# Optimization experiments

Hardware: AMD Instinct MI355X
Metric: run time of the kernel (lower is better)

Reference implementation:

```python
import jax, jax.numpy as jnp
import numpy as np

B, T, C = 4, 2048, 1024
H = 16
D = C // H  # head_dim = 64

def setup_inputs() -> dict:
    key = jax.random.key(0)
    k1, k2, k3 = jax.random.split(key, 3)
    s = 1.0 / np.sqrt(C)
    x = jax.random.normal(k1, (B, T, C), dtype=jnp.float32)
    w_qkv = jax.random.normal(k2, (C, 3 * C), dtype=jnp.float32) * s
    w_proj = jax.random.normal(k3, (C, C), dtype=jnp.float32) * s
    b_proj = jnp.zeros((C,), dtype=jnp.float32)
    return {"x": x, "w_qkv": w_qkv, "w_proj": w_proj, "b_proj": b_proj}

def reference(x, w_qkv, w_proj, b_proj):
    Bc, Tc, Cc = x.shape
    scale = 1.0 / np.sqrt(D)
    qkv = x @ w_qkv                       # [B,T,3C]
    q, k, v = jnp.split(qkv, 3, axis=-1)  # each [B,T,C]
    def heads(t):
        return t.reshape(Bc, Tc, H, D).transpose(0, 2, 1, 3)  # [B,H,T,D]
    q, k, v = heads(q), heads(k), heads(v)
    attn = jnp.einsum('bhqd,bhkd->bhqk', q, k) * scale        # [B,H,T,T]
    causal = jnp.tril(jnp.ones((Tc, Tc), dtype=bool))
    attn = jnp.where(causal, attn, -jnp.inf)
    attn = jax.nn.softmax(attn, axis=-1)
    out = jnp.einsum('bhqk,bhkd->bhqd', attn, v)              # [B,H,T,D]
    out = out.transpose(0, 2, 1, 3).reshape(Bc, Tc, Cc)
    return out @ w_proj + b_proj
```

## Files before the change

### kernel.cpp

```cpp
#include <hip/hip_runtime.h>

typedef unsigned short u16;
typedef unsigned int u32;
typedef __attribute__((ext_vector_type(8))) __bf16 bf16x8;
typedef __attribute__((ext_vector_type(4))) float f32x4;
typedef __attribute__((ext_vector_type(16))) float f32x16;
typedef __attribute__((ext_vector_type(8))) unsigned short ushort8;
typedef __attribute__((ext_vector_type(4))) unsigned short ushort4v;
typedef __attribute__((ext_vector_type(4))) unsigned int u32x4;
typedef __attribute__((ext_vector_type(4))) float float4v;

#define B_ 4
#define T_ 2048
#define C_ 1024
#define H_ 16
#define D_ 64
#define M_ (B_ * T_)

union ABUn { ushort8 u; bf16x8 b; };

__device__ __forceinline__ u16 f2bf(float f) {
  u32 u = __builtin_bit_cast(u32, f);
  u32 r = u + 0x7fffu + ((u >> 16) & 1u);
  return (u16)(r >> 16);
}

__device__ __forceinline__ float fexp2(float x) {
  float r; asm("v_exp_f32 %0, %1" : "=v"(r) : "v"(x)); return r;
}

__device__ __forceinline__ u32 pkbf(float lo, float hi_) {
  u32 r; asm("v_cvt_pk_bf16_f32 %0, %1, %2" : "=v"(r) : "v"(lo), "v"(hi_)); return r;
}

__device__ __forceinline__ void gl16(const u16* g, u16* l) {
  __builtin_amdgcn_global_load_lds((const __attribute__((address_space(1))) void*)g,
                                   (__attribute__((address_space(3))) void*)l, 16, 0, 0);
}

__global__ void cast_kernel(const float* __restrict__ in, u16* __restrict__ out, int n4) {
  int i = blockIdx.x * blockDim.x + threadIdx.x;
  if (i >= n4) return;
  float4v v = ((const float4v*)in)[i];
  ushort4v o;
  o[0] = f2bf(v[0]); o[1] = f2bf(v[1]); o[2] = f2bf(v[2]); o[3] = f2bf(v[3]);
  ((ushort4v*)out)[i] = o;
}

__global__ void transpose_cast_kernel(const float* __restrict__ src, u16* __restrict__ dst,
                                      int Kd, int Nd) {
  __shared__ float tile[32][33];
  int n0 = blockIdx.x * 32, k0 = blockIdx.y * 32;
  int tx = threadIdx.x, ty = threadIdx.y;
#pragma unroll
  for (int i = 0; i < 32; i += 8)
    tile[ty + i][tx] = src[(k0 + ty + i) * Nd + n0 + tx];
  __syncthreads();
#pragma unroll
  for (int i = 0; i < 32; i += 8)
    dst[(n0 + ty + i) * Kd + k0 + tx] = f2bf(tile[tx][ty + i]);
}

template <int EPI>
__global__ __launch_bounds__(256, 2) void gemm_bt(
    const u16* __restrict__ A, const u16* __restrict__ Bt,
    u16* __restrict__ Qb, u16* __restrict__ Kb, u16* __restrict__ Vb,
    float* __restrict__ Out, const float* __restrict__ bias) {
  __shared__ u16 As[128 * 64];
  __shared__ u16 Bs[128 * 64];
  const int tid = threadIdx.x;
  const int lane = tid & 63, wave = tid >> 6;
  const int wm = wave >> 1, wn = wave & 1;
  const int lg = lane >> 4, lr = lane & 15;
  const int m0 = blockIdx.y * 128, n0 = blockIdx.x * 128;

  f32x4 acc[4][4];
  const f32x4 zero = {0.0f, 0.0f, 0.0f, 0.0f};
#pragma unroll
  for (int mi = 0; mi < 4; ++mi)
#pragma unroll
    for (int ni = 0; ni < 4; ++ni) acc[mi][ni] = zero;

  const u16* Abase = A + m0 * 1024;
  const u16* Bbase = Bt + n0 * 1024;
  int aoff[4];
#pragma unroll
  for (int j = 0; j < 4; ++j) {
    int s = wave * 256 + j * 64 + lane;
    int row = s >> 3, sp = s & 7;
    aoff[j] = row * 1024 + (sp ^ (row & 7)) * 8;
  }
  char* AsB = (char*)As;
  char* BsB = (char*)Bs;

  for (int k0 = 0; k0 < 1024; k0 += 64) {
#pragma unroll
    for (int j = 0; j < 4; ++j) {
      u16* ldst_a = &As[(wave * 256 + j * 64) * 8];
      u16* ldst_b = &Bs[(wave * 256 + j * 64) * 8];
      gl16(Abase + aoff[j] + k0, ldst_a);
      gl16(Bbase + aoff[j] + k0, ldst_b);
    }
    __syncthreads();
#pragma unroll
    for (int kk = 0; kk < 2; ++kk) {
      bf16x8 am[4], bn[4];
#pragma unroll
      for (int mi = 0; mi < 4; ++mi) {
        int row = wm * 64 + mi * 16 + lr;
        ABUn u;
        u.u = *(const ushort8*)(AsB + ((u32)(row * 128 + ((kk * 64 + lg * 16) ^ ((row & 7) << 4)))));
        am[mi] = u.b;
      }
#pragma unroll
      for (int ni = 0; ni < 4; ++ni) {
        int row = wn * 64 + ni * 16 + lr;
        ABUn u;
        u.u = *(const ushort8*)(BsB + ((u32)(row * 128 + ((kk * 64 + lg * 16) ^ ((row & 7) << 4)))));
        bn[ni] = u.b;
      }
#pragma unroll
      for (int mi = 0; mi < 4; ++mi)
#pragma unroll
        for (int ni = 0; ni < 4; ++ni)
          acc[mi][ni] = __builtin_amdgcn_mfma_f32_16x16x32_bf16(am[mi], bn[ni], acc[mi][ni], 0, 0, 0);
    }
    __syncthreads();
  }

#pragma unroll
  for (int mi = 0; mi < 4; ++mi)
#pragma unroll
    for (int ni = 0; ni < 4; ++ni) {
      int m = m0 + wm * 64 + mi * 16 + lg * 4;
      int n = n0 + wn * 64 + ni * 16 + lr;
      if (EPI == 0) {
        int part = n >> 10, c = n & 1023;
        int h = c >> 6, d = c & 63;
        int b = m >> 11, t = m & 2047;
        if (part == 2) {
          ushort4v pv;
#pragma unroll
          for (int r = 0; r < 4; ++r) pv[r] = f2bf(acc[mi][ni][r]);
          *(ushort4v*)&Vb[((b * H_ + h) * D_ + d) * T_ + t] = pv;
        } else {
#pragma unroll
          for (int r = 0; r < 4; ++r) {
            float v = acc[mi][ni][r];
            if (part == 0)
              Qb[((b * H_ + h) * T_ + t + r) * D_ + d] = f2bf(v * 0.18033688f);
            else
              Kb[((b * H_ + h) * T_ + t + r) * D_ + d] = f2bf(v);
          }
        }
      } else {
#pragma unroll
        for (int r = 0; r < 4; ++r)
          Out[(m + r) * 1024 + n] = acc[mi][ni][r] + bias[n];
      }
    }
}

__global__ __launch_bounds__(256, 2) void attn_kernel(
    const u16* __restrict__ Qb, const u16* __restrict__ Kb,
    const u16* __restrict__ Vt, u16* __restrict__ Ob) {
  __shared__ u16 smem[4][4096];
  const int bh = blockIdx.y;
  const int q0 = (7 - (int)blockIdx.x) * 256;
  const int tid = threadIdx.x;
  const int lane = tid & 63, wave = tid >> 6;
  const int hi = lane >> 5, ln = lane & 31;
  const int qw0 = q0 + wave * 64;
  const int hh = bh & (H_ - 1), bb = bh >> 4;

  const u16* Qh = Qb + bh * (T_ * D_);
  const u16* Kh = Kb + bh * (T_ * D_);
  const u16* Vh = Vt + bh * (T_ * D_);

  bf16x8 qf[2][4];
#pragma unroll
  for (int qt = 0; qt < 2; ++qt) {
    const u16* qr = Qh + (qw0 + qt * 32 + ln) * 64 + hi * 8;
#pragma unroll
    for (int ks = 0; ks < 4; ++ks)
      qf[qt][ks] = __builtin_bit_cast(bf16x8, *(const ushort8*)(qr + ks * 16));
  }

  f32x16 o[2][2];
#pragma unroll
  for (int dt = 0; dt < 2; ++dt)
#pragma unroll
    for (int qt = 0; qt < 2; ++qt)
#pragma unroll
      for (int i = 0; i < 16; ++i) o[dt][qt][i] = 0.0f;
  float m[2] = {-1e30f, -1e30f}, l[2] = {0.0f, 0.0f};

  const int nchunk = q0 / 64 + 4;
  const int slot0 = wave * 128;

#pragma unroll
  for (int j = 0; j < 2; ++j) {
    int slot = slot0 + j * 64 + lane;
    int r = slot >> 3, sp = slot & 7;
    int sl = sp ^ (r & 7);
    gl16(Kh + r * 64 + sl * 8, &smem[0][(slot0 + j * 64) * 8]);
    gl16(Vh + r * 2048 + sl * 8, &smem[2][(slot0 + j * 64) * 8]);
  }
  __syncthreads();

  for (int ch = 0; ch < nchunk; ++ch) {
    const int kv0 = ch * 64;
    const int cur = ch & 1;
    if (ch + 1 < nchunk) {
      const int kn = kv0 + 64;
#pragma unroll
      for (int j = 0; j < 2; ++j) {
        int slot = slot0 + j * 64 + lane;
        int r = slot >> 3, sp = slot & 7;
        int sl = sp ^ (r & 7);
        gl16(Kh + (kn + r) * 64 + sl * 8, &smem[cur ^ 1][(slot0 + j * 64) * 8]);
        gl16(Vh + r * 2048 + kn + sl * 8, &smem[2 + (cur ^ 1)][(slot0 + j * 64) * 8]);
      }
    }
    if (kv0 <= qw0 + 63) {
      const char* Kc = (const char*)smem[cur];
      const char* Vc = (const char*)smem[2 + cur];
      bf16x8 kf[2][4];
#pragma unroll
      for (int sub = 0; sub < 2; ++sub) {
        int r = sub * 32 + ln;
        u32 rs = (u32)((r & 7) << 4);
#pragma unroll
        for (int ks = 0; ks < 4; ++ks)
          kf[sub][ks] = __builtin_bit_cast(bf16x8,
              *(const ushort8*)(Kc + r * 128 + (u32)((ks * 32 + hi * 16) ^ rs)));
      }
      const bool partial = (kv0 + 63) > qw0;
      bf16x8 pb[2][4];
#pragma unroll
      for (int qt = 0; qt < 2; ++qt) {
        f32x16 s0, s1;
#pragma unroll
        for (int i = 0; i < 16; ++i) { s0[i] = 0.0f; s1[i] = 0.0f; }
#pragma unroll
        for (int ks = 0; ks < 4; ++ks) {
          s0 = __builtin_amdgcn_mfma_f32_32x32x16_bf16(kf[0][ks], qf[qt][ks], s0, 0, 0, 0);
          s1 = __builtin_amdgcn_mfma_f32_32x32x16_bf16(kf[1][ks], qf[qt][ks], s1, 0, 0, 0);
        }
        const int qg = qw0 + qt * 32 + ln;
        if (partial) {
#pragma unroll
          for (int r = 0; r < 16; ++r) {
            int R = (r & 3) + 8 * (r >> 2) + 4 * hi;
            s0[r] = (kv0 + R > qg) ? -1e30f : s0[r];
            s1[r] = (kv0 + 32 + R > qg) ? -1e30f : s1[r];
          }
        }
        float cm = -1e30f;
#pragma unroll
        for (int r = 0; r < 16; ++r) cm = fmaxf(cm, fmaxf(s0[r], s1[r]));
        cm = fmaxf(cm, __shfl_xor(cm, 32));
        float mn = fmaxf(m[qt], cm);
        float fsc = fexp2(m[qt] - mn);
        m[qt] = mn;
        float ssum = 0.0f;
#pragma unroll
        for (int r = 0; r < 16; ++r) {
          s0[r] = fexp2(s0[r] - mn);
          s1[r] = fexp2(s1[r] - mn);
          ssum += s0[r] + s1[r];
        }
        ssum += __shfl_xor(ssum, 32);
        l[qt] = l[qt] * fsc + ssum;
#pragma unroll
        for (int dt = 0; dt < 2; ++dt)
#pragma unroll
          for (int i = 0; i < 16; ++i) o[dt][qt][i] *= fsc;
#pragma unroll
        for (int sub = 0; sub < 2; ++sub) {
          u32 a0, a1, a2, a3, a4, a5, a6, a7;
          if (sub == 0) {
            a0 = pkbf(s0[0], s0[1]);  a1 = pkbf(s0[2], s0[3]);
            a2 = pkbf(s0[4], s0[5]);  a3 = pkbf(s0[6], s0[7]);
            a4 = pkbf(s0[8], s0[9]);  a5 = pkbf(s0[10], s0[11]);
            a6 = pkbf(s0[12], s0[13]); a7 = pkbf(s0[14], s0[15]);
          } else {
            a0 = pkbf(s1[0], s1[1]);  a1 = pkbf(s1[2], s1[3]);
            a2 = pkbf(s1[4], s1[5]);  a3 = pkbf(s1[6], s1[7]);
            a4 = pkbf(s1[8], s1[9]);  a5 = pkbf(s1[10], s1[11]);
            a6 = pkbf(s1[12], s1[13]); a7 = pkbf(s1[14], s1[15]);
          }
          u32 x0 = __shfl_xor(hi ? a0 : a2, 32);
          u32 x1 = __shfl_xor(hi ? a1 : a3, 32);
          u32 x2 = __shfl_xor(hi ? a4 : a6, 32);
          u32 x3 = __shfl_xor(hi ? a5 : a7, 32);
          u32x4 w0, w1;
          w0[0] = hi ? x0 : a0; w0[1] = hi ? x1 : a1;
          w0[2] = hi ? a2 : x0; w0[3] = hi ? a3 : x1;
          w1[0] = hi ? x2 : a4; w1[1] = hi ? x3 : a5;
          w1[2] = hi ? a6 : x2; w1[3] = hi ? a7 : x3;
          pb[qt][sub * 2 + 0] = __builtin_bit_cast(bf16x8, w0);
          pb[qt][sub * 2 + 1] = __builtin_bit_cast(bf16x8, w1);
        }
      }
#pragma unroll
      for (int dt = 0; dt < 2; ++dt) {
        int r = dt * 32 + ln;
        u32 rs = (u32)((r & 7) << 4);
#pragma unroll
        for (int ks = 0; ks < 4; ++ks) {
          bf16x8 vfk = __builtin_bit_cast(bf16x8,
              *(const ushort8*)(Vc + r * 128 + (u32)((ks * 32 + hi * 16) ^ rs)));
#pragma unroll
          for (int qt = 0; qt < 2; ++qt)
            o[dt][qt] = __builtin_amdgcn_mfma_f32_32x32x16_bf16(vfk, pb[qt][ks], o[dt][qt], 0, 0, 0);
        }
      }
    }
    __syncthreads();
  }

  __syncthreads();
  char* Wb = (char*)smem[wave];
#pragma unroll
  for (int qt = 0; qt < 2; ++qt) {
    float inv = 1.0f / l[qt];
    int q = qt * 32 + ln;
    u32 rs = (u32)((q & 7) << 4);
#pragma unroll
    for (int dt = 0; dt < 2; ++dt)
#pragma unroll
      for (int p = 0; p < 8; ++p) {
        u32 w = pkbf(o[dt][qt][2 * p] * inv, o[dt][qt][2 * p + 1] * inv);
        int d = dt * 32 + ((2 * p) & 3) + 8 * (p >> 1) + 4 * hi;
        *(u32*)(Wb + ((u32)(q * 128 + d * 2) ^ rs)) = w;
      }
  }
#pragma unroll
  for (int j = 0; j < 8; ++j) {
    int idx = j * 64 + lane;
    int row = idx >> 3, sp = idx & 7;
    ushort8 v = *(const ushort8*)(Wb + row * 128 + (u32)((sp * 16) ^ ((row & 7) << 4)));
    *(ushort8*)(Ob + (bb * T_ + qw0 + row) * C_ + hh * 64 + sp * 8) = v;
  }
}

extern "C" void kernel_launch(void* const* d_in, const int* in_sizes, int n_in,
                              void* d_out, int out_size, void* d_ws, size_t ws_size,
                              hipStream_t stream) {
  const float* x = (const float*)d_in[0];
  const float* w_qkv = (const float*)d_in[1];
  const float* w_proj = (const float*)d_in[2];
  const float* b_proj = (const float*)d_in[3];
  float* out = (float*)d_out;

  char* ws = (char*)d_ws;
  u16* xb = (u16*)(ws);
  u16* wqT = (u16*)(ws + 16777216);
  u16* wpT = (u16*)(ws + 16777216 + 6291456);
  u16* Qb = (u16*)(ws + 25165824);
  u16* Kb = (u16*)(ws + 25165824 + 16777216);
  u16* Vt = (u16*)(ws + 25165824 + 2 * 16777216);
  u16* Ob = xb;

  cast_kernel<<<(M_ * C_ / 4 + 255) / 256, 256, 0, stream>>>(x, xb, M_ * C_ / 4);
  dim3 tb(32, 8);
  transpose_cast_kernel<<<dim3(3 * C_ / 32, C_ / 32), tb, 0, stream>>>(w_qkv, wqT, C_, 3 * C_);
  transpose_cast_kernel<<<dim3(C_ / 32, C_ / 32), tb, 0, stream>>>(w_proj, wpT, C_, C_);

  gemm_bt<0><<<dim3(3 * C_ / 128, M_ / 128), 256, 0, stream>>>(
      xb, wqT, Qb, Kb, Vt, nullptr, nullptr);

  attn_kernel<<<dim3(T_ / 256, B_ * H_), 256, 0, stream>>>(Qb, Kb, Vt, Ob);

  gemm_bt<1><<<dim3(C_ / 128, M_ / 128), 256, 0, stream>>>(
      Ob, wpT, nullptr, nullptr, nullptr, out, b_proj);
}
```

Baseline: 283.1 us.

## Shrink attention query tile to 128 rows per block, one 32-row tile per wave

The attention kernel now gives each block 128 query rows (32 per wave) instead of 256, doubling the grid and halving per-wave accumulators and registers so that four blocks per CU can be resident. K fragments are loaded inside the MFMA loop instead of being held in registers, MFMA sections are wrapped in s_setprio, and the max and sum reductions are done as trees. The goal is better occupancy and load balance across the causal work, at the cost of each block re-reading K/V more times per query row.

```diff
diff --git a/kernel.cpp b/kernel.cpp
--- a/kernel.cpp
+++ b/kernel.cpp
@@ -161,41 +161,38 @@
     }
 }
 
-__global__ __launch_bounds__(256, 2) void attn_kernel(
+__global__ __launch_bounds__(256, 4) void attn_kernel(
     const u16* __restrict__ Qb, const u16* __restrict__ Kb,
     const u16* __restrict__ Vt, u16* __restrict__ Ob) {
   __shared__ u16 smem[4][4096];
   const int bh = blockIdx.y;
-  const int q0 = (7 - (int)blockIdx.x) * 256;
+  const int q0 = (15 - (int)blockIdx.x) * 128;
   const int tid = threadIdx.x;
   const int lane = tid & 63, wave = tid >> 6;
   const int hi = lane >> 5, ln = lane & 31;
-  const int qw0 = q0 + wave * 64;
+  const int qw0 = q0 + wave * 32;
   const int hh = bh & (H_ - 1), bb = bh >> 4;
 
   const u16* Qh = Qb + bh * (T_ * D_);
   const u16* Kh = Kb + bh * (T_ * D_);
   const u16* Vh = Vt + bh * (T_ * D_);
 
-  bf16x8 qf[2][4];
-#pragma unroll
-  for (int qt = 0; qt < 2; ++qt) {
-    const u16* qr = Qh + (qw0 + qt * 32 + ln) * 64 + hi * 8;
+  bf16x8 qf[4];
+  {
+    const u16* qr = Qh + (qw0 + ln) * 64 + hi * 8;
 #pragma unroll
     for (int ks = 0; ks < 4; ++ks)
-      qf[qt][ks] = __builtin_bit_cast(bf16x8, *(const ushort8*)(qr + ks * 16));
-  }
-
-  f32x16 o[2][2];
+      qf[ks] = __builtin_bit_cast(bf16x8, *(const ushort8*)(qr + ks * 16));
+  }
+
+  f32x16 o[2];
 #pragma unroll
   for (int dt = 0; dt < 2; ++dt)
 #pragma unroll
-    for (int qt = 0; qt < 2; ++qt)
-#pragma unroll
-      for (int i = 0; i < 16; ++i) o[dt][qt][i] = 0.0f;
-  float m[2] = {-1e30f, -1e30f}, l[2] = {0.0f, 0.0f};
-
-  const int nchunk = q0 / 64 + 4;
+    for (int i = 0; i < 16; ++i) o[dt][i] = 0.0f;
+  float m = -1e30f, l = 0.0f;
+
+  const int nchunk = q0 / 64 + 2;
   const int slot0 = wave * 128;
 
 #pragma unroll
@@ -222,87 +219,91 @@
         gl16(Vh + r * 2048 + kn + sl * 8, &smem[2 + (cur ^ 1)][(slot0 + j * 64) * 8]);
       }
     }
-    if (kv0 <= qw0 + 63) {
+    if (kv0 <= qw0 + 31) {
       const char* Kc = (const char*)smem[cur];
       const char* Vc = (const char*)smem[2 + cur];
-      bf16x8 kf[2][4];
+      f32x16 s0, s1;
+#pragma unroll
+      for (int i = 0; i < 16; ++i) { s0[i] = 0.0f; s1[i] = 0.0f; }
+      __builtin_amdgcn_s_setprio(1);
+#pragma unroll
+      for (int ks = 0; ks < 4; ++ks) {
+        int r0 = ln, r1 = 32 + ln;
+        bf16x8 kf0 = __builtin_bit_cast(bf16x8,
+            *(const ushort8*)(Kc + r0 * 128 + (u32)((ks * 32 + hi * 16) ^ ((r0 & 7) << 4))));
+        bf16x8 kf1 = __builtin_bit_cast(bf16x8,
+            *(const ushort8*)(Kc + r1 * 128 + (u32)((ks * 32 + hi * 16) ^ ((r1 & 7) << 4))));
+        s0 = __builtin_amdgcn_mfma_f32_32x32x16_bf16(kf0, qf[ks], s0, 0, 0, 0);
+        s1 = __builtin_amdgcn_mfma_f32_32x32x16_bf16(kf1, qf[ks], s1, 0, 0, 0);
+      }
+      __builtin_amdgcn_s_setprio(0);
+
+      const int qg = qw0 + ln;
+      if ((kv0 + 63) > qw0) {
+#pragma unroll
+        for (int r = 0; r < 16; ++r) {
+          int R = (r & 3) + 8 * (r >> 2) + 4 * hi;
+          s0[r] = (kv0 + R > qg) ? -1e30f : s0[r];
+          s1[r] = (kv0 + 32 + R > qg) ? -1e30f : s1[r];
+        }
+      }
+      float mx[8];
+#pragma unroll
+      for (int i = 0; i < 8; ++i)
+        mx[i] = fmaxf(fmaxf(s0[i], s0[i + 8]), fmaxf(s1[i], s1[i + 8]));
+#pragma unroll
+      for (int i = 0; i < 4; ++i) mx[i] = fmaxf(mx[i], mx[i + 4]);
+      float cm = fmaxf(fmaxf(mx[0], mx[1]), fmaxf(mx[2], mx[3]));
+      cm = fmaxf(cm, __shfl_xor(cm, 32));
+      float mn = fmaxf(m, cm);
+      float fsc = fexp2(m - mn);
+      m = mn;
+#pragma unroll
+      for (int r = 0; r < 16; ++r) {
+        s0[r] = fexp2(s0[r] - mn);
+        s1[r] = fexp2(s1[r] - mn);
+      }
+      float sm[8];
+#pragma unroll
+      for (int i = 0; i < 8; ++i) sm[i] = (s0[i] + s0[i + 8]) + (s1[i] + s1[i + 8]);
+#pragma unroll
+      for (int i = 0; i < 4; ++i) sm[i] += sm[i + 4];
+      float ssum = (sm[0] + sm[1]) + (sm[2] + sm[3]);
+      ssum += __shfl_xor(ssum, 32);
+      l = l * fsc + ssum;
+#pragma unroll
+      for (int dt = 0; dt < 2; ++dt)
+#pragma unroll
+        for (int i = 0; i < 16; ++i) o[dt][i] *= fsc;
+
+      bf16x8 pb[4];
 #pragma unroll
       for (int sub = 0; sub < 2; ++sub) {
-        int r = sub * 32 + ln;
-        u32 rs = (u32)((r & 7) << 4);
-#pragma unroll
-        for (int ks = 0; ks < 4; ++ks)
-          kf[sub][ks] = __builtin_bit_cast(bf16x8,
-              *(const ushort8*)(Kc + r * 128 + (u32)((ks * 32 + hi * 16) ^ rs)));
-      }
-      const bool partial = (kv0 + 63) > qw0;
-      bf16x8 pb[2][4];
-#pragma unroll
-      for (int qt = 0; qt < 2; ++qt) {
-        f32x16 s0, s1;
-#pragma unroll
-        for (int i = 0; i < 16; ++i) { s0[i] = 0.0f; s1[i] = 0.0f; }
-#pragma unroll
-        for (int ks = 0; ks < 4; ++ks) {
-          s0 = __builtin_amdgcn_mfma_f32_32x32x16_bf16(kf[0][ks], qf[qt][ks], s0, 0, 0, 0);
-          s1 = __builtin_amdgcn_mfma_f32_32x32x16_bf16(kf[1][ks], qf[qt][ks], s1, 0, 0, 0);
+        u32 a0, a1, a2, a3, a4, a5, a6, a7;
+        if (sub == 0) {
+          a0 = pkbf(s0[0], s0[1]);  a1 = pkbf(s0[2], s0[3]);
+          a2 = pkbf(s0[4], s0[5]);  a3 = pkbf(s0[6], s0[7]);
+          a4 = pkbf(s0[8], s0[9]);  a5 = pkbf(s0[10], s0[11]);
+          a6 = pkbf(s0[12], s0[13]); a7 = pkbf(s0[14], s0[15]);
+        } else {
+          a0 = pkbf(s1[0], s1[1]);  a1 = pkbf(s1[2], s1[3]);
+          a2 = pkbf(s1[4], s1[5]);  a3 = pkbf(s1[6], s1[7]);
+          a4 = pkbf(s1[8], s1[9]);  a5 = pkbf(s1[10], s1[11]);
+          a6 = pkbf(s1[12], s1[13]); a7 = pkbf(s1[14], s1[15]);
         }
-        const int qg = qw0 + qt * 32 + ln;
-        if (partial) {
-#pragma unroll
-          for (int r = 0; r < 16; ++r) {
-            int R = (r & 3) + 8 * (r >> 2) + 4 * hi;
-            s0[r] = (kv0 + R > qg) ? -1e30f : s0[r];
-            s1[r] = (kv0 + 32 + R > qg) ? -1e30f : s1[r];
-          }
-        }
-        float cm = -1e30f;
-#pragma unroll
-        for (int r = 0; r < 16; ++r) cm = fmaxf(cm, fmaxf(s0[r], s1[r]));
-        cm = fmaxf(cm, __shfl_xor(cm, 32));
-        float mn = fmaxf(m[qt], cm);
-        float fsc = fexp2(m[qt] - mn);
-        m[qt] = mn;
-        float ssum = 0.0f;
-#pragma unroll
-        for (int r = 0; r < 16; ++r) {
-          s0[r] = fexp2(s0[r] - mn);
-          s1[r] = fexp2(s1[r] - mn);
-          ssum += s0[r] + s1[r];
-        }
-        ssum += __shfl_xor(ssum, 32);
-        l[qt] = l[qt] * fsc + ssum;
-#pragma unroll
-        for (int dt = 0; dt < 2; ++dt)
-#pragma unroll
-          for (int i = 0; i < 16; ++i) o[dt][qt][i] *= fsc;
-#pragma unroll
-        for (int sub = 0; sub < 2; ++sub) {
-          u32 a0, a1, a2, a3, a4, a5, a6, a7;
-          if (sub == 0) {
-            a0 = pkbf(s0[0], s0[1]);  a1 = pkbf(s0[2], s0[3]);
-            a2 = pkbf(s0[4], s0[5]);  a3 = pkbf(s0[6], s0[7]);
-            a4 = pkbf(s0[8], s0[9]);  a5 = pkbf(s0[10], s0[11]);
-            a6 = pkbf(s0[12], s0[13]); a7 = pkbf(s0[14], s0[15]);
-          } else {
-            a0 = pkbf(s1[0], s1[1]);  a1 = pkbf(s1[2], s1[3]);
-            a2 = pkbf(s1[4], s1[5]);  a3 = pkbf(s1[6], s1[7]);
-            a4 = pkbf(s1[8], s1[9]);  a5 = pkbf(s1[10], s1[11]);
-            a6 = pkbf(s1[12], s1[13]); a7 = pkbf(s1[14], s1[15]);
-          }
-          u32 x0 = __shfl_xor(hi ? a0 : a2, 32);
-          u32 x1 = __shfl_xor(hi ? a1 : a3, 32);
-          u32 x2 = __shfl_xor(hi ? a4 : a6, 32);
-          u32 x3 = __shfl_xor(hi ? a5 : a7, 32);
-          u32x4 w0, w1;
-          w0[0] = hi ? x0 : a0; w0[1] = hi ? x1 : a1;
-          w0[2] = hi ? a2 : x0; w0[3] = hi ? a3 : x1;
-          w1[0] = hi ? x2 : a4; w1[1] = hi ? x3 : a5;
-          w1[2] = hi ? a6 : x2; w1[3] = hi ? a7 : x3;
-          pb[qt][sub * 2 + 0] = __builtin_bit_cast(bf16x8, w0);
-          pb[qt][sub * 2 + 1] = __builtin_bit_cast(bf16x8, w1);
-        }
-      }
+        u32 x0 = __shfl_xor(hi ? a0 : a2, 32);
+        u32 x1 = __shfl_xor(hi ? a1 : a3, 32);
+        u32 x2 = __shfl_xor(hi ? a4 : a6, 32);
+        u32 x3 = __shfl_xor(hi ? a5 : a7, 32);
+        u32x4 w0, w1;
+        w0[0] = hi ? x0 : a0; w0[1] = hi ? x1 : a1;
+        w0[2] = hi ? a2 : x0; w0[3] = hi ? a3 : x1;
+        w1[0] = hi ? x2 : a4; w1[1] = hi ? x3 : a5;
+        w1[2] = hi ? a6 : x2; w1[3] = hi ? a7 : x3;
+        pb[sub * 2 + 0] = __builtin_bit_cast(bf16x8, w0);
+        pb[sub * 2 + 1] = __builtin_bit_cast(bf16x8, w1);
+      }
+      __builtin_amdgcn_s_setprio(1);
 #pragma unroll
       for (int dt = 0; dt < 2; ++dt) {
         int r = dt * 32 + ln;
@@ -311,33 +312,31 @@
         for (int ks = 0; ks < 4; ++ks) {
           bf16x8 vfk = __builtin_bit_cast(bf16x8,
               *(const ushort8*)(Vc + r * 128 + (u32)((ks * 32 + hi * 16) ^ rs)));
-#pragma unroll
-          for (int qt = 0; qt < 2; ++qt)
-            o[dt][qt] = __builtin_amdgcn_mfma_f32_32x32x16_bf16(vfk, pb[qt][ks], o[dt][qt], 0, 0, 0);
+          o[dt] = __builtin_amdgcn_mfma_f32_32x32x16_bf16(vfk, pb[ks], o[dt], 0, 0, 0);
         }
       }
+      __builtin_amdgcn_s_setprio(0);
     }
     __syncthreads();
   }
 
   __syncthreads();
   char* Wb = (char*)smem[wave];
-#pragma unroll
-  for (int qt = 0; qt < 2; ++qt) {
-    float inv = 1.0f / l[qt];
-    int q = qt * 32 + ln;
+  {
+    float inv = 1.0f / l;
+    int q = ln;
     u32 rs = (u32)((q & 7) << 4);
 #pragma unroll
     for (int dt = 0; dt < 2; ++dt)
 #pragma unroll
       for (int p = 0; p < 8; ++p) {
-        u32 w = pkbf(o[dt][qt][2 * p] * inv, o[dt][qt][2 * p + 1] * inv);
+        u32 w = pkbf(o[dt][2 * p] * inv, o[dt][2 * p + 1] * inv);
         int d = dt * 32 + ((2 * p) & 3) + 8 * (p >> 1) + 4 * hi;
         *(u32*)(Wb + ((u32)(q * 128 + d * 2) ^ rs)) = w;
       }
   }
 #pragma unroll
-  for (int j = 0; j < 8; ++j) {
+  for (int j = 0; j < 4; ++j) {
     int idx = j * 64 + lane;
     int row = idx >> 3, sp = idx & 7;
     ushort8 v = *(const ushort8*)(Wb + row * 128 + (u32)((sp * 16) ^ ((row & 7) << 4)));
@@ -371,7 +370,7 @@
   gemm_bt<0><<<dim3(3 * C_ / 128, M_ / 128), 256, 0, stream>>>(
       xb, wqT, Qb, Kb, Vt, nullptr, nullptr);
 
-  attn_kernel<<<dim3(T_ / 256, B_ * H_), 256, 0, stream>>>(Qb, Kb, Vt, Ob);
+  attn_kernel<<<dim3(T_ / 128, B_ * H_), 256, 0, stream>>>(Qb, Kb, Vt, Ob);
 
   gemm_bt<1><<<dim3(C_ / 128, M_ / 128), 256, 0, stream>>>(
       Ob, wpT, nullptr, nullptr, nullptr, out, b_proj);
```

After: 280.6 us. Within noise of the previous version (-0.9%).
